# Performance work log

Measured on AMD Instinct MI355X. Metric: run time of the kernel, lower is better.

## Reference

```python
import jax, jax.numpy as jnp
import numpy as np

N = 50000      # nodes
E = 800000     # edges (before self-loops)
HEADS = 4
IN = 128
HID = 96
DH = HID // HEADS  # 24 per-head channels
G = 64         # graphs in batch
OUT = 3


def setup_inputs() -> dict:
    key = jax.random.key(0)
    ks = jax.random.split(key, 16)
    def w(k, shape, fan):
        return (jax.random.normal(k, shape, jnp.float32) * (fan ** -0.5)).astype(jnp.float32)
    x = jax.random.normal(ks[0], (N, IN), jnp.float32)
    edge_index = jax.random.randint(ks[1], (2, E), 0, N, dtype=jnp.int32)
    batch = jnp.sort(jax.random.randint(ks[2], (N,), 0, G, dtype=jnp.int32))
    return {
        'x': x, 'edge_index': edge_index, 'batch': batch, 'num_graphs': G,
        'W1': w(ks[3], (IN, HID), IN),
        'att_src1': w(ks[4], (HEADS, DH), DH),
        'att_dst1': w(ks[5], (HEADS, DH), DH),
        'b1': jnp.zeros((HID,), jnp.float32),
        'W2': w(ks[6], (HID, HID), HID),
        'att_src2': w(ks[7], (HEADS, DH), DH),
        'att_dst2': w(ks[8], (HEADS, DH), DH),
        'b2': jnp.zeros((HID,), jnp.float32),
        'g_w1': w(ks[9], (HID, HID // 2), HID),
        'g_b1': jnp.zeros((HID // 2,), jnp.float32),
        'g_w2': w(ks[10], (HID // 2, 1), HID // 2),
        'g_b2': jnp.zeros((1,), jnp.float32),
        'f_w1': w(ks[11], (HID, HID), HID),
        'f_b1': jnp.zeros((HID,), jnp.float32),
        'f_w2': w(ks[12], (HID, OUT), HID),
        'f_b2': jnp.zeros((OUT,), jnp.float32),
    }


def _gat_layer(x, src, dst, W, a_src, a_dst, b, n):
    # x: [n, F]; src/dst: [E'] (self-loops included). PyG GATConv math.
    h = (x @ W).reshape(n, HEADS, DH)                 # [n, H, d]
    alpha_s = jnp.sum(h * a_src[None], axis=-1)       # [n, H]
    alpha_d = jnp.sum(h * a_dst[None], axis=-1)       # [n, H]
    e = jax.nn.leaky_relu(alpha_s[src] + alpha_d[dst], 0.2)  # [E', H]
    # segment softmax over incoming edges of each dst node
    m = jax.ops.segment_max(e, dst, num_segments=n)   # [n, H]
    ex = jnp.exp(e - m[dst])
    denom = jax.ops.segment_sum(ex, dst, num_segments=n)
    alpha = ex / (denom[dst] + 1e-16)                 # [E', H]
    msg = h[src] * alpha[:, :, None]                  # [E', H, d]
    out = jax.ops.segment_sum(msg, dst, num_segments=n)
    return out.reshape(n, HEADS * DH) + b


def reference(x, edge_index, batch, num_graphs, W1, att_src1, att_dst1, b1,
              W2, att_src2, att_dst2, b2, g_w1, g_b1, g_w2, g_b2,
              f_w1, f_b1, f_w2, f_b2):
    n = x.shape[0]
    loops = jnp.arange(n, dtype=edge_index.dtype)
    src = jnp.concatenate([edge_index[0], loops])     # add self-loops (PyG default)
    dst = jnp.concatenate([edge_index[1], loops])
    h = jax.nn.elu(_gat_layer(x, src, dst, W1, att_src1, att_dst1, b1, n))
    h = jax.nn.elu(_gat_layer(h, src, dst, W2, att_src2, att_dst2, b2, n))
    # GlobalAttention pool: gate_nn -> softmax over batch segments -> weighted sum
    gate = (jax.nn.relu(h @ g_w1 + g_b1) @ g_w2 + g_b2)[:, 0]   # [n]
    gm = jax.ops.segment_max(gate, batch, num_segments=num_graphs)
    gm = jnp.where(jnp.isfinite(gm), gm, 0.0)
    ge = jnp.exp(gate - gm[batch])
    gden = jax.ops.segment_sum(ge, batch, num_segments=num_graphs)
    wgt = ge / (gden[batch] + 1e-16)                  # [n]
    pooled = jax.ops.segment_sum(h * wgt[:, None], batch, num_segments=num_graphs)  # [G, HID]
    return jax.nn.relu(pooled @ f_w1 + f_b1) @ f_w2 + f_b2   # [G, 3]
```

## Files before the change

kernel.cpp:

```cpp
#include <hip/hip_runtime.h>
#include <cmath>

typedef unsigned int uint32;

__device__ __forceinline__ uint32 pack_bf16x2(float a, float b) {
    uint32 ua = __float_as_uint(a), ub = __float_as_uint(b);
    ua = (ua + 0x7fffu + ((ua >> 16) & 1u)) >> 16;
    ub = (ub + 0x7fffu + ((ub >> 16) & 1u)) >> 16;
    return ua | (ub << 16);
}

template<int K, int NCOL, int TN, int MODE>
__device__ __forceinline__ void gemm_body(int bid, const float* __restrict__ X,
                                          const float* __restrict__ W,
                                          const float* __restrict__ v1,
                                          const float* __restrict__ v2,
                                          const float* __restrict__ v3,
                                          uint32* __restrict__ H16, float* __restrict__ Hf,
                                          float* __restrict__ AS, float* __restrict__ AD,
                                          int n_nodes) {
    const int t = threadIdx.x;
    const int tx = t & 15, ty = t >> 4;
    const int c0 = tx * TN;
    const int m0 = ty * 4;
    const int node0 = bid * 64;

    __shared__ float As[16][68];
    __shared__ float Bs[16][NCOL];

    float acc[4][TN];
#pragma unroll
    for (int i = 0; i < 4; i++)
#pragma unroll
        for (int j = 0; j < TN; j++) acc[i][j] = 0.f;

    const int am = t >> 2, akq = t & 3;

    for (int kb = 0; kb < K; kb += 16) {
        float4 av = make_float4(0.f, 0.f, 0.f, 0.f);
        int anode = node0 + am;
        if (anode < n_nodes)
            av = *reinterpret_cast<const float4*>(X + (size_t)anode * K + kb + akq * 4);
        As[akq * 4 + 0][am] = av.x;
        As[akq * 4 + 1][am] = av.y;
        As[akq * 4 + 2][am] = av.z;
        As[akq * 4 + 3][am] = av.w;
        {
            const float4* wsrc = reinterpret_cast<const float4*>(W + (size_t)kb * NCOL);
            float4* bdst = reinterpret_cast<float4*>(&Bs[0][0]);
            for (int i = t; i < 16 * NCOL / 4; i += 256) bdst[i] = wsrc[i];
        }
        __syncthreads();
#pragma unroll
        for (int k = 0; k < 16; k++) {
            float4 a4 = *reinterpret_cast<const float4*>(&As[k][m0]);
            float a[4] = {a4.x, a4.y, a4.z, a4.w};
            float b[TN];
            if constexpr ((TN & 1) == 0) {
#pragma unroll
                for (int j = 0; j < TN / 2; j++) {
                    float2 b2 = *reinterpret_cast<const float2*>(&Bs[k][c0 + 2 * j]);
                    b[2 * j] = b2.x; b[2 * j + 1] = b2.y;
                }
            } else {
#pragma unroll
                for (int j = 0; j < TN; j++) b[j] = Bs[k][c0 + j];
            }
#pragma unroll
            for (int i = 0; i < 4; i++)
#pragma unroll
                for (int j = 0; j < TN; j++)
                    acc[i][j] = fmaf(a[i], b[j], acc[i][j]);
        }
        __syncthreads();
    }

    if constexpr (MODE == 0) {
        __shared__ float s_as[64][16];
        __shared__ float s_ad[64][16];
#pragma unroll
        for (int i = 0; i < 4; i++) {
            int node = node0 + m0 + i;
            float asp = 0.f, adp = 0.f;
#pragma unroll
            for (int j = 0; j < TN; j++) {
                asp = fmaf(acc[i][j], v1[c0 + j], asp);
                adp = fmaf(acc[i][j], v2[c0 + j], adp);
            }
            s_as[m0 + i][tx] = asp;
            s_ad[m0 + i][tx] = adp;
            if (node < n_nodes) {
#pragma unroll
                for (int j = 0; j < TN / 2; j++) {
                    H16[(size_t)node * 48 + tx * (TN / 2) + j] =
                        pack_bf16x2(acc[i][2 * j], acc[i][2 * j + 1]);
                }
            }
        }
        __syncthreads();
        int m = t >> 2, head = t & 3;
        int node = node0 + m;
        if (node < n_nodes) {
            float s1 = s_as[m][head * 4 + 0] + s_as[m][head * 4 + 1]
                     + s_as[m][head * 4 + 2] + s_as[m][head * 4 + 3];
            float s2 = s_ad[m][head * 4 + 0] + s_ad[m][head * 4 + 1]
                     + s_ad[m][head * 4 + 2] + s_ad[m][head * 4 + 3];
            AS[(size_t)node * 4 + head] = s1;
            AD[(size_t)node * 4 + head] = s2;
        }
    } else {
        __shared__ float s_g[64][16];
#pragma unroll
        for (int i = 0; i < 4; i++) {
            float p = 0.f;
#pragma unroll
            for (int j = 0; j < TN; j++) {
                float a = acc[i][j] + v1[c0 + j];
                a = fmaxf(a, 0.f);
                p = fmaf(a, v2[c0 + j], p);
            }
            s_g[m0 + i][tx] = p;
        }
        __syncthreads();
        if (t < 64) {
            int node = node0 + t;
            if (node < n_nodes) {
                float s = 0.f;
#pragma unroll
                for (int j = 0; j < 16; j++) s += s_g[t][j];
                Hf[node] = s + v3[0];
            }
        }
    }
}

template<int K, int NCOL, int TN, int MODE>
__global__ __launch_bounds__(256)
void tiled_gemm_kernel(const float* __restrict__ X, const float* __restrict__ W,
                       const float* __restrict__ v1, const float* __restrict__ v2,
                       const float* __restrict__ v3,
                       uint32* __restrict__ H16, float* __restrict__ Hf,
                       float* __restrict__ AS, float* __restrict__ AD, int n_nodes) {
    gemm_body<K, NCOL, TN, MODE>(blockIdx.x, X, W, v1, v2, v3, H16, Hf, AS, AD, n_nodes);
}

template<int K, int NCOL, int TN>
__global__ __launch_bounds__(256)
void gemm_hist_kernel(const float* __restrict__ X, const float* __restrict__ W,
                      const float* __restrict__ v1, const float* __restrict__ v2,
                      uint32* __restrict__ H16, float* __restrict__ AS, float* __restrict__ AD,
                      int n_nodes, int nb_gemm,
                      const int* __restrict__ dst, int* __restrict__ deg, int E) {
    if ((int)blockIdx.x < nb_gemm) {
        gemm_body<K, NCOL, TN, 0>(blockIdx.x, X, W, v1, v2, nullptr, H16, nullptr,
                                  AS, AD, n_nodes);
    } else {
        int tid = (blockIdx.x - nb_gemm) * 256 + threadIdx.x;
        int stride = (gridDim.x - nb_gemm) * 256;
        for (int e = tid; e < E; e += stride) atomicAdd(&deg[dst[e]], 1);
    }
}

__global__ void scan_bsum_kernel(const int* __restrict__ deg, int* __restrict__ bsum, int n) {
    __shared__ int s[256];
    int t = threadIdx.x;
    int base = blockIdx.x * 1024;
    int sum = 0;
#pragma unroll
    for (int j = 0; j < 4; j++) {
        int i = base + j * 256 + t;
        if (i < n) sum += deg[i] + 1;
    }
    s[t] = sum;
    __syncthreads();
    for (int off = 128; off; off >>= 1) {
        if (t < off) s[t] += s[t + off];
        __syncthreads();
    }
    if (t == 0) bsum[blockIdx.x] = s[0];
}

__global__ void scan_local_kernel(const int* __restrict__ deg, const int* __restrict__ bsum,
                                  int nb, int* __restrict__ rowptr, int* __restrict__ pos,
                                  int n) {
    __shared__ int s[256];
    __shared__ int boff[257];
    int t = threadIdx.x;
    if (t < nb) boff[t] = bsum[t];
    __syncthreads();
    if (t == 0) {
        int run = 0;
        for (int i = 0; i < nb; i++) { int v = boff[i]; boff[i] = run; run += v; }
        boff[nb] = run;
    }
    __syncthreads();
    if (blockIdx.x == 0 && t == 0) rowptr[n] = boff[nb];

    int base = blockIdx.x * 1024;
    int d[4];
    int sum = 0;
#pragma unroll
    for (int j = 0; j < 4; j++) {
        int i = base + t * 4 + j;
        d[j] = (i < n) ? deg[i] + 1 : 0;
        sum += d[j];
    }
    s[t] = sum;
    __syncthreads();
    for (int off = 1; off < 256; off <<= 1) {
        int x = (t >= off) ? s[t - off] : 0;
        __syncthreads();
        s[t] += x;
        __syncthreads();
    }
    int run = boff[blockIdx.x] + s[t] - sum;
#pragma unroll
    for (int j = 0; j < 4; j++) {
        int i = base + t * 4 + j;
        if (i < n) { rowptr[i] = run; pos[i] = run; }
        run += d[j];
    }
}

__global__ void fill_kernel(const int* __restrict__ src, const int* __restrict__ dst,
                            int* __restrict__ pos, int* __restrict__ col, int E, int N) {
    int i = blockIdx.x * blockDim.x + threadIdx.x;
    if (i < E) {
        int p = atomicAdd(&pos[dst[i]], 1);
        col[p] = src[i];
    } else if (i < E + N) {
        int n = i - E;
        int p = atomicAdd(&pos[n], 1);
        col[p] = n;
    }
}

__global__ __launch_bounds__(256)
void gat_gather_kernel(const uint32* __restrict__ H16, const float* __restrict__ AS,
                       const float* __restrict__ AD, const int* __restrict__ rowptr,
                       const int* __restrict__ col, const float* __restrict__ bias,
                       float* __restrict__ OUT, int n_nodes) {
    int wid = threadIdx.x >> 6, lane = threadIdx.x & 63;
    int n = blockIdx.x * 4 + wid;
    if (n >= n_nodes) return;
    int beg = rowptr[n], end = rowptr[n + 1];

    int h = lane & 3, slot = lane >> 2;
    float ad_n = AD[(size_t)n * 4 + h];

    int c = lane;
    bool cown = c < 48;
    int head_c = cown ? (c / 12) : 0;
    const uint32* __restrict__ Hc = H16 + c;

    float denom = 0.f;
    float2 acc0 = make_float2(0.f, 0.f), acc1 = make_float2(0.f, 0.f);
    float2 acc2 = make_float2(0.f, 0.f), acc3 = make_float2(0.f, 0.f);
    float2 acc4 = make_float2(0.f, 0.f), acc5 = make_float2(0.f, 0.f);
    float2 acc6 = make_float2(0.f, 0.f), acc7 = make_float2(0.f, 0.f);

    for (int base = beg; base < end; base += 16) {
        int ce = base + slot;
        int s_e = 0;
        float ex = 0.f;
        if (ce < end) {
            s_e = col[ce];
            float v = AS[(size_t)s_e * 4 + h] + ad_n;
            v = v > 0.f ? v : 0.2f * v;
            ex = __expf(v);
        }
        denom += ex;
        int cnt = end - base;

        int sbv[16];
        float wv[16];
#pragma unroll
        for (int i = 0; i < 16; i++) {
            sbv[i] = __shfl(s_e, i * 4, 64);
            wv[i]  = __shfl(ex,  i * 4 + head_c, 64);
        }

#pragma unroll
        for (int g = 0; g < 16; g += 8) {
            if (g < cnt && cown) {
                uint32 u0 = Hc[(size_t)sbv[g + 0] * 48];
                uint32 u1 = Hc[(size_t)sbv[g + 1] * 48];
                uint32 u2 = Hc[(size_t)sbv[g + 2] * 48];
                uint32 u3 = Hc[(size_t)sbv[g + 3] * 48];
                uint32 u4 = Hc[(size_t)sbv[g + 4] * 48];
                uint32 u5 = Hc[(size_t)sbv[g + 5] * 48];
                uint32 u6 = Hc[(size_t)sbv[g + 6] * 48];
                uint32 u7 = Hc[(size_t)sbv[g + 7] * 48];
                acc0.x = fmaf(__uint_as_float(u0 << 16), wv[g + 0], acc0.x);
                acc0.y = fmaf(__uint_as_float(u0 & 0xffff0000u), wv[g + 0], acc0.y);
                acc1.x = fmaf(__uint_as_float(u1 << 16), wv[g + 1], acc1.x);
                acc1.y = fmaf(__uint_as_float(u1 & 0xffff0000u), wv[g + 1], acc1.y);
                acc2.x = fmaf(__uint_as_float(u2 << 16), wv[g + 2], acc2.x);
                acc2.y = fmaf(__uint_as_float(u2 & 0xffff0000u), wv[g + 2], acc2.y);
                acc3.x = fmaf(__uint_as_float(u3 << 16), wv[g + 3], acc3.x);
                acc3.y = fmaf(__uint_as_float(u3 & 0xffff0000u), wv[g + 3], acc3.y);
                acc4.x = fmaf(__uint_as_float(u4 << 16), wv[g + 4], acc4.x);
                acc4.y = fmaf(__uint_as_float(u4 & 0xffff0000u), wv[g + 4], acc4.y);
                acc5.x = fmaf(__uint_as_float(u5 << 16), wv[g + 5], acc5.x);
                acc5.y = fmaf(__uint_as_float(u5 & 0xffff0000u), wv[g + 5], acc5.y);
                acc6.x = fmaf(__uint_as_float(u6 << 16), wv[g + 6], acc6.x);
                acc6.y = fmaf(__uint_as_float(u6 & 0xffff0000u), wv[g + 6], acc6.y);
                acc7.x = fmaf(__uint_as_float(u7 << 16), wv[g + 7], acc7.x);
                acc7.y = fmaf(__uint_as_float(u7 & 0xffff0000u), wv[g + 7], acc7.y);
            }
        }
    }

#pragma unroll
    for (int m = 4; m <= 32; m <<= 1)
        denom += __shfl_xor(denom, m, 64);
    float den = __shfl(denom, head_c, 64);

    if (cown) {
        float2 a;
        a.x = ((acc0.x + acc1.x) + (acc2.x + acc3.x)) + ((acc4.x + acc5.x) + (acc6.x + acc7.x));
        a.y = ((acc0.y + acc1.y) + (acc2.y + acc3.y)) + ((acc4.y + acc5.y) + (acc6.y + acc7.y));
        float2 b2 = reinterpret_cast<const float2*>(bias)[c];
        float inv = 1.f / (den + 1e-16f);
        float ox = a.x * inv + b2.x;
        float oy = a.y * inv + b2.y;
        ox = ox > 0.f ? ox : (__expf(ox) - 1.f);
        oy = oy > 0.f ? oy : (__expf(oy) - 1.f);
        reinterpret_cast<float2*>(OUT)[(size_t)n * 48 + c] = make_float2(ox, oy);
    }
}

__global__ __launch_bounds__(384)
void pool_accum_kernel(const float* __restrict__ H2, const float* __restrict__ gate,
                       const int* __restrict__ batch, int n_nodes,
                       float* __restrict__ pooled, float* __restrict__ denp) {
    const int NPB = 256;
    int t = threadIdx.x;
    int group = t / 96;
    int c = t - group * 96;
    if (group >= 4) return;
    int nbeg = blockIdx.x * NPB;
    int nend = min(nbeg + NPB, n_nodes);

    float acc = 0.f, dacc = 0.f;
    int curg = -1;
    for (int i = nbeg + group; i < nend; i += 4) {
        int g = batch[i];
        if (g != curg) {
            if (curg >= 0) {
                atomicAdd(&pooled[(size_t)curg * 96 + c], acc);
                if (c == 0) atomicAdd(&denp[curg], dacc);
            }
            acc = 0.f; dacc = 0.f;
            curg = g;
        }
        float ge = __expf(gate[i]);
        acc = fmaf(ge, H2[(size_t)i * 96 + c], acc);
        if (c == 0) dacc += ge;
    }
    if (curg >= 0) {
        atomicAdd(&pooled[(size_t)curg * 96 + c], acc);
        if (c == 0) atomicAdd(&denp[curg], dacc);
    }
}

__global__ void final_kernel(const float* __restrict__ pooled, const float* __restrict__ denp,
                             const float* __restrict__ f_w1, const float* __restrict__ f_b1,
                             const float* __restrict__ f_w2, const float* __restrict__ f_b2,
                             float* __restrict__ out) {
    int g = blockIdx.x, t = threadIdx.x;
    __shared__ float sp[96], sh[96];
    sp[t] = pooled[(size_t)g * 96 + t] / (denp[g] + 1e-16f);
    __syncthreads();
    float a = f_b1[t];
    for (int k = 0; k < 96; k++) a = fmaf(sp[k], f_w1[k * 96 + t], a);
    sh[t] = fmaxf(a, 0.f);
    __syncthreads();
    if (t < 3) {
        float o = f_b2[t];
        for (int k = 0; k < 96; k++) o = fmaf(sh[k], f_w2[k * 3 + t], o);
        out[g * 3 + t] = o;
    }
}

extern "C" void kernel_launch(void* const* d_in, const int* in_sizes, int n_in,
                              void* d_out, int out_size, void* d_ws, size_t ws_size,
                              hipStream_t stream) {
    const float* x    = (const float*)d_in[0];
    const int*   ei   = (const int*)d_in[1];
    const int*   batch= (const int*)d_in[2];
    const float* W1   = (const float*)d_in[4];
    const float* as1  = (const float*)d_in[5];
    const float* ad1  = (const float*)d_in[6];
    const float* b1   = (const float*)d_in[7];
    const float* W2   = (const float*)d_in[8];
    const float* as2  = (const float*)d_in[9];
    const float* ad2  = (const float*)d_in[10];
    const float* b2   = (const float*)d_in[11];
    const float* g_w1 = (const float*)d_in[12];
    const float* g_b1 = (const float*)d_in[13];
    const float* g_w2 = (const float*)d_in[14];
    const float* g_b2 = (const float*)d_in[15];
    const float* f_w1 = (const float*)d_in[16];
    const float* f_b1 = (const float*)d_in[17];
    const float* f_w2 = (const float*)d_in[18];
    const float* f_b2 = (const float*)d_in[19];
    float* out = (float*)d_out;

    int N = in_sizes[0] / 128;
    int E = in_sizes[1] / 2;
    int G = out_size / 3;
    const int* srcv = ei;
    const int* dstv = ei + E;

    char* base = (char*)d_ws;
    int*   deg    = (int*)base;
    float* pooled = (float*)(base + (size_t)N * 4);
    float* denp   = (float*)(base + (size_t)N * 4 + (size_t)G * 96 * 4);
    size_t zbytes = (size_t)(N + G * 96 + G) * 4;

    char* p = base + ((zbytes + 255) & ~(size_t)255);
    auto alloc = [&](size_t bytes) {
        char* q = p;
        p += (bytes + 255) & ~(size_t)255;
        return q;
    };
    uint32* hA   = (uint32*)alloc((size_t)N * 48 * 4);
    float* hB    = (float*)alloc((size_t)N * 96 * 4);
    float* AS    = (float*)alloc((size_t)N * 4 * 4);
    float* AD    = (float*)alloc((size_t)N * 4 * 4);
    float* gatev = (float*)alloc((size_t)N * 4);
    int*   pos   = (int*)alloc((size_t)N * 4);
    int*   rowptr= (int*)alloc(((size_t)N + 1) * 4);
    int*   bsum  = (int*)alloc((size_t)256 * 4);
    int*   col   = (int*)alloc((size_t)(E + N) * 4);

    const int B = 256;
    int gemm_blocks = (N + 63) / 64;
    int nb_scan = (N + 1023) / 1024;

    hipMemsetAsync(base, 0, zbytes, stream);

    gemm_hist_kernel<128, 96, 6><<<gemm_blocks + 256, 256, 0, stream>>>(
        x, W1, as1, ad1, hA, AS, AD, N, gemm_blocks, dstv, deg, E);

    scan_bsum_kernel<<<nb_scan, 256, 0, stream>>>(deg, bsum, N);
    scan_local_kernel<<<nb_scan, 256, 0, stream>>>(deg, bsum, nb_scan, rowptr, pos, N);
    fill_kernel<<<(E + N + B - 1) / B, B, 0, stream>>>(srcv, dstv, pos, col, E, N);

    gat_gather_kernel<<<(N + 3) / 4, 256, 0, stream>>>(hA, AS, AD, rowptr, col, b1, hB, N);
    tiled_gemm_kernel<96, 96, 6, 0><<<gemm_blocks, 256, 0, stream>>>(
        hB, W2, as2, ad2, nullptr, hA, nullptr, AS, AD, N);
    gat_gather_kernel<<<(N + 3) / 4, 256, 0, stream>>>(hA, AS, AD, rowptr, col, b2, hB, N);

    tiled_gemm_kernel<96, 48, 3, 1><<<gemm_blocks, 256, 0, stream>>>(
        hB, g_w1, g_b1, g_w2, g_b2, nullptr, gatev, nullptr, nullptr, N);
    pool_accum_kernel<<<(N + 255) / 256, 384, 0, stream>>>(
        hB, gatev, batch, N, pooled, denp);
    final_kernel<<<G, 96, 0, stream>>>(pooled, denp, f_w1, f_b1, f_w2, f_b2, out);
}
```

Baseline: 302.0 us.

## Fuse gate MLP into second GAT gather and widen per-lane feature loads

The separate gate GEMM kernel is removed. Its 96x48 MLP, ReLU and dot-product reduction now run per node inside the second gather kernel, reading the node's output row from shared memory, which saves a kernel launch and a re-read of the hidden matrix. The gather is also reorganised so each lane loads 8 bytes (4 bf16 channels) per edge, with lane pairs splitting even and odd edges and combining their sums by a shuffle. The trade-off is that the fused gate costs each wave a serial 96-step loop with uncoalesced-per-lane loads of gW1 on every node, which may lengthen the gather kernel.

```diff
diff --git a/kernel.cpp b/kernel.cpp
--- a/kernel.cpp
+++ b/kernel.cpp
@@ -10,13 +10,12 @@
     return ua | (ub << 16);
 }
 
-template<int K, int NCOL, int TN, int MODE>
+template<int K, int NCOL, int TN>
 __device__ __forceinline__ void gemm_body(int bid, const float* __restrict__ X,
                                           const float* __restrict__ W,
                                           const float* __restrict__ v1,
                                           const float* __restrict__ v2,
-                                          const float* __restrict__ v3,
-                                          uint32* __restrict__ H16, float* __restrict__ Hf,
+                                          uint32* __restrict__ H16,
                                           float* __restrict__ AS, float* __restrict__ AD,
                                           int n_nodes) {
     const int t = threadIdx.x;
@@ -56,15 +55,10 @@
             float4 a4 = *reinterpret_cast<const float4*>(&As[k][m0]);
             float a[4] = {a4.x, a4.y, a4.z, a4.w};
             float b[TN];
-            if constexpr ((TN & 1) == 0) {
-#pragma unroll
-                for (int j = 0; j < TN / 2; j++) {
-                    float2 b2 = *reinterpret_cast<const float2*>(&Bs[k][c0 + 2 * j]);
-                    b[2 * j] = b2.x; b[2 * j + 1] = b2.y;
-                }
-            } else {
-#pragma unroll
-                for (int j = 0; j < TN; j++) b[j] = Bs[k][c0 + j];
+#pragma unroll
+            for (int j = 0; j < TN / 2; j++) {
+                float2 b2 = *reinterpret_cast<const float2*>(&Bs[k][c0 + 2 * j]);
+                b[2 * j] = b2.x; b[2 * j + 1] = b2.y;
             }
 #pragma unroll
             for (int i = 0; i < 4; i++)
@@ -75,73 +69,47 @@
         __syncthreads();
     }
 
-    if constexpr (MODE == 0) {
-        __shared__ float s_as[64][16];
-        __shared__ float s_ad[64][16];
-#pragma unroll
-        for (int i = 0; i < 4; i++) {
-            int node = node0 + m0 + i;
-            float asp = 0.f, adp = 0.f;
-#pragma unroll
-            for (int j = 0; j < TN; j++) {
-                asp = fmaf(acc[i][j], v1[c0 + j], asp);
-                adp = fmaf(acc[i][j], v2[c0 + j], adp);
+    __shared__ float s_as[64][16];
+    __shared__ float s_ad[64][16];
+#pragma unroll
+    for (int i = 0; i < 4; i++) {
+        int node = node0 + m0 + i;
+        float asp = 0.f, adp = 0.f;
+#pragma unroll
+        for (int j = 0; j < TN; j++) {
+            asp = fmaf(acc[i][j], v1[c0 + j], asp);
+            adp = fmaf(acc[i][j], v2[c0 + j], adp);
+        }
+        s_as[m0 + i][tx] = asp;
+        s_ad[m0 + i][tx] = adp;
+        if (node < n_nodes) {
+#pragma unroll
+            for (int j = 0; j < TN / 2; j++) {
+                H16[(size_t)node * 48 + tx * (TN / 2) + j] =
+                    pack_bf16x2(acc[i][2 * j], acc[i][2 * j + 1]);
             }
-            s_as[m0 + i][tx] = asp;
-            s_ad[m0 + i][tx] = adp;
-            if (node < n_nodes) {
-#pragma unroll
-                for (int j = 0; j < TN / 2; j++) {
-                    H16[(size_t)node * 48 + tx * (TN / 2) + j] =
-                        pack_bf16x2(acc[i][2 * j], acc[i][2 * j + 1]);
-                }
-            }
-        }
-        __syncthreads();
-        int m = t >> 2, head = t & 3;
-        int node = node0 + m;
-        if (node < n_nodes) {
-            float s1 = s_as[m][head * 4 + 0] + s_as[m][head * 4 + 1]
-                     + s_as[m][head * 4 + 2] + s_as[m][head * 4 + 3];
-            float s2 = s_ad[m][head * 4 + 0] + s_ad[m][head * 4 + 1]
-                     + s_ad[m][head * 4 + 2] + s_ad[m][head * 4 + 3];
-            AS[(size_t)node * 4 + head] = s1;
-            AD[(size_t)node * 4 + head] = s2;
-        }
-    } else {
-        __shared__ float s_g[64][16];
-#pragma unroll
-        for (int i = 0; i < 4; i++) {
-            float p = 0.f;
-#pragma unroll
-            for (int j = 0; j < TN; j++) {
-                float a = acc[i][j] + v1[c0 + j];
-                a = fmaxf(a, 0.f);
-                p = fmaf(a, v2[c0 + j], p);
-            }
-            s_g[m0 + i][tx] = p;
-        }
-        __syncthreads();
-        if (t < 64) {
-            int node = node0 + t;
-            if (node < n_nodes) {
-                float s = 0.f;
-#pragma unroll
-                for (int j = 0; j < 16; j++) s += s_g[t][j];
-                Hf[node] = s + v3[0];
-            }
-        }
-    }
-}
-
-template<int K, int NCOL, int TN, int MODE>
+        }
+    }
+    __syncthreads();
+    int m = t >> 2, head = t & 3;
+    int node = node0 + m;
+    if (node < n_nodes) {
+        float s1 = s_as[m][head * 4 + 0] + s_as[m][head * 4 + 1]
+                 + s_as[m][head * 4 + 2] + s_as[m][head * 4 + 3];
+        float s2 = s_ad[m][head * 4 + 0] + s_ad[m][head * 4 + 1]
+                 + s_ad[m][head * 4 + 2] + s_ad[m][head * 4 + 3];
+        AS[(size_t)node * 4 + head] = s1;
+        AD[(size_t)node * 4 + head] = s2;
+    }
+}
+
+template<int K, int NCOL, int TN>
 __global__ __launch_bounds__(256)
 void tiled_gemm_kernel(const float* __restrict__ X, const float* __restrict__ W,
                        const float* __restrict__ v1, const float* __restrict__ v2,
-                       const float* __restrict__ v3,
-                       uint32* __restrict__ H16, float* __restrict__ Hf,
-                       float* __restrict__ AS, float* __restrict__ AD, int n_nodes) {
-    gemm_body<K, NCOL, TN, MODE>(blockIdx.x, X, W, v1, v2, v3, H16, Hf, AS, AD, n_nodes);
+                       uint32* __restrict__ H16, float* __restrict__ AS,
+                       float* __restrict__ AD, int n_nodes) {
+    gemm_body<K, NCOL, TN>(blockIdx.x, X, W, v1, v2, H16, AS, AD, n_nodes);
 }
 
 template<int K, int NCOL, int TN>
@@ -152,8 +120,7 @@
                       int n_nodes, int nb_gemm,
                       const int* __restrict__ dst, int* __restrict__ deg, int E) {
     if ((int)blockIdx.x < nb_gemm) {
-        gemm_body<K, NCOL, TN, 0>(blockIdx.x, X, W, v1, v2, nullptr, H16, nullptr,
-                                  AS, AD, n_nodes);
+        gemm_body<K, NCOL, TN>(blockIdx.x, X, W, v1, v2, H16, AS, AD, n_nodes);
     } else {
         int tid = (blockIdx.x - nb_gemm) * 256 + threadIdx.x;
         int stride = (gridDim.x - nb_gemm) * 256;
@@ -235,11 +202,16 @@
     }
 }
 
+template<bool GATE>
 __global__ __launch_bounds__(256)
 void gat_gather_kernel(const uint32* __restrict__ H16, const float* __restrict__ AS,
                        const float* __restrict__ AD, const int* __restrict__ rowptr,
                        const int* __restrict__ col, const float* __restrict__ bias,
-                       float* __restrict__ OUT, int n_nodes) {
+                       float* __restrict__ OUT, int n_nodes,
+                       const float* __restrict__ gW1, const float* __restrict__ gb1,
+                       const float* __restrict__ gw2, const float* __restrict__ gb2,
+                       float* __restrict__ gatev) {
+    __shared__ float sh_h[4][96];
     int wid = threadIdx.x >> 6, lane = threadIdx.x & 63;
     int n = blockIdx.x * 4 + wid;
     if (n >= n_nodes) return;
@@ -248,16 +220,13 @@
     int h = lane & 3, slot = lane >> 2;
     float ad_n = AD[(size_t)n * 4 + h];
 
-    int c = lane;
-    bool cown = c < 48;
-    int head_c = cown ? (c / 12) : 0;
-    const uint32* __restrict__ Hc = H16 + c;
+    int pe = lane & 1, q = lane >> 1;
+    bool cown = lane < 48;
+    int head_q = cown ? (q / 6) : 0;
+    const uint2* __restrict__ Hq = reinterpret_cast<const uint2*>(H16) + (cown ? q : 0);
 
     float denom = 0.f;
-    float2 acc0 = make_float2(0.f, 0.f), acc1 = make_float2(0.f, 0.f);
-    float2 acc2 = make_float2(0.f, 0.f), acc3 = make_float2(0.f, 0.f);
-    float2 acc4 = make_float2(0.f, 0.f), acc5 = make_float2(0.f, 0.f);
-    float2 acc6 = make_float2(0.f, 0.f), acc7 = make_float2(0.f, 0.f);
+    float4 acc0 = make_float4(0.f, 0.f, 0.f, 0.f), acc1 = acc0, acc2 = acc0, acc3 = acc0;
 
     for (int base = beg; base < end; base += 16) {
         int ce = base + slot;
@@ -272,41 +241,38 @@
         denom += ex;
         int cnt = end - base;
 
-        int sbv[16];
-        float wv[16];
-#pragma unroll
-        for (int i = 0; i < 16; i++) {
-            sbv[i] = __shfl(s_e, i * 4, 64);
-            wv[i]  = __shfl(ex,  i * 4 + head_c, 64);
-        }
-
-#pragma unroll
-        for (int g = 0; g < 16; g += 8) {
-            if (g < cnt && cown) {
-                uint32 u0 = Hc[(size_t)sbv[g + 0] * 48];
-                uint32 u1 = Hc[(size_t)sbv[g + 1] * 48];
-                uint32 u2 = Hc[(size_t)sbv[g + 2] * 48];
-                uint32 u3 = Hc[(size_t)sbv[g + 3] * 48];
-                uint32 u4 = Hc[(size_t)sbv[g + 4] * 48];
-                uint32 u5 = Hc[(size_t)sbv[g + 5] * 48];
-                uint32 u6 = Hc[(size_t)sbv[g + 6] * 48];
-                uint32 u7 = Hc[(size_t)sbv[g + 7] * 48];
-                acc0.x = fmaf(__uint_as_float(u0 << 16), wv[g + 0], acc0.x);
-                acc0.y = fmaf(__uint_as_float(u0 & 0xffff0000u), wv[g + 0], acc0.y);
-                acc1.x = fmaf(__uint_as_float(u1 << 16), wv[g + 1], acc1.x);
-                acc1.y = fmaf(__uint_as_float(u1 & 0xffff0000u), wv[g + 1], acc1.y);
-                acc2.x = fmaf(__uint_as_float(u2 << 16), wv[g + 2], acc2.x);
-                acc2.y = fmaf(__uint_as_float(u2 & 0xffff0000u), wv[g + 2], acc2.y);
-                acc3.x = fmaf(__uint_as_float(u3 << 16), wv[g + 3], acc3.x);
-                acc3.y = fmaf(__uint_as_float(u3 & 0xffff0000u), wv[g + 3], acc3.y);
-                acc4.x = fmaf(__uint_as_float(u4 << 16), wv[g + 4], acc4.x);
-                acc4.y = fmaf(__uint_as_float(u4 & 0xffff0000u), wv[g + 4], acc4.y);
-                acc5.x = fmaf(__uint_as_float(u5 << 16), wv[g + 5], acc5.x);
-                acc5.y = fmaf(__uint_as_float(u5 & 0xffff0000u), wv[g + 5], acc5.y);
-                acc6.x = fmaf(__uint_as_float(u6 << 16), wv[g + 6], acc6.x);
-                acc6.y = fmaf(__uint_as_float(u6 & 0xffff0000u), wv[g + 6], acc6.y);
-                acc7.x = fmaf(__uint_as_float(u7 << 16), wv[g + 7], acc7.x);
-                acc7.y = fmaf(__uint_as_float(u7 & 0xffff0000u), wv[g + 7], acc7.y);
+        int sb[8];
+        float w[8];
+#pragma unroll
+        for (int j = 0; j < 8; j++) {
+            int esel = 2 * j + pe;
+            sb[j] = __shfl(s_e, esel * 4, 64);
+            w[j]  = __shfl(ex,  esel * 4 + head_q, 64);
+        }
+
+#pragma unroll
+        for (int g = 0; g < 8; g += 4) {
+            if (2 * g < cnt && cown) {
+                uint2 u0 = Hq[(size_t)sb[g + 0] * 24];
+                uint2 u1 = Hq[(size_t)sb[g + 1] * 24];
+                uint2 u2 = Hq[(size_t)sb[g + 2] * 24];
+                uint2 u3 = Hq[(size_t)sb[g + 3] * 24];
+                acc0.x = fmaf(__uint_as_float(u0.x << 16),        w[g + 0], acc0.x);
+                acc0.y = fmaf(__uint_as_float(u0.x & 0xffff0000u), w[g + 0], acc0.y);
+                acc0.z = fmaf(__uint_as_float(u0.y << 16),        w[g + 0], acc0.z);
+                acc0.w = fmaf(__uint_as_float(u0.y & 0xffff0000u), w[g + 0], acc0.w);
+                acc1.x = fmaf(__uint_as_float(u1.x << 16),        w[g + 1], acc1.x);
+                acc1.y = fmaf(__uint_as_float(u1.x & 0xffff0000u), w[g + 1], acc1.y);
+                acc1.z = fmaf(__uint_as_float(u1.y << 16),        w[g + 1], acc1.z);
+                acc1.w = fmaf(__uint_as_float(u1.y & 0xffff0000u), w[g + 1], acc1.w);
+                acc2.x = fmaf(__uint_as_float(u2.x << 16),        w[g + 2], acc2.x);
+                acc2.y = fmaf(__uint_as_float(u2.x & 0xffff0000u), w[g + 2], acc2.y);
+                acc2.z = fmaf(__uint_as_float(u2.y << 16),        w[g + 2], acc2.z);
+                acc2.w = fmaf(__uint_as_float(u2.y & 0xffff0000u), w[g + 2], acc2.w);
+                acc3.x = fmaf(__uint_as_float(u3.x << 16),        w[g + 3], acc3.x);
+                acc3.y = fmaf(__uint_as_float(u3.x & 0xffff0000u), w[g + 3], acc3.y);
+                acc3.z = fmaf(__uint_as_float(u3.y << 16),        w[g + 3], acc3.z);
+                acc3.w = fmaf(__uint_as_float(u3.y & 0xffff0000u), w[g + 3], acc3.w);
             }
         }
     }
@@ -314,19 +280,48 @@
 #pragma unroll
     for (int m = 4; m <= 32; m <<= 1)
         denom += __shfl_xor(denom, m, 64);
-    float den = __shfl(denom, head_c, 64);
-
-    if (cown) {
-        float2 a;
-        a.x = ((acc0.x + acc1.x) + (acc2.x + acc3.x)) + ((acc4.x + acc5.x) + (acc6.x + acc7.x));
-        a.y = ((acc0.y + acc1.y) + (acc2.y + acc3.y)) + ((acc4.y + acc5.y) + (acc6.y + acc7.y));
-        float2 b2 = reinterpret_cast<const float2*>(bias)[c];
+    float den = __shfl(denom, head_q, 64);
+
+    float4 a;
+    a.x = (acc0.x + acc1.x) + (acc2.x + acc3.x);
+    a.y = (acc0.y + acc1.y) + (acc2.y + acc3.y);
+    a.z = (acc0.z + acc1.z) + (acc2.z + acc3.z);
+    a.w = (acc0.w + acc1.w) + (acc2.w + acc3.w);
+    a.x += __shfl_xor(a.x, 1, 64);
+    a.y += __shfl_xor(a.y, 1, 64);
+    a.z += __shfl_xor(a.z, 1, 64);
+    a.w += __shfl_xor(a.w, 1, 64);
+
+    if (cown && pe == 0) {
         float inv = 1.f / (den + 1e-16f);
-        float ox = a.x * inv + b2.x;
-        float oy = a.y * inv + b2.y;
-        ox = ox > 0.f ? ox : (__expf(ox) - 1.f);
-        oy = oy > 0.f ? oy : (__expf(oy) - 1.f);
-        reinterpret_cast<float2*>(OUT)[(size_t)n * 48 + c] = make_float2(ox, oy);
+        float4 b4 = reinterpret_cast<const float4*>(bias)[q];
+        float4 o;
+        o.x = a.x * inv + b4.x;
+        o.y = a.y * inv + b4.y;
+        o.z = a.z * inv + b4.z;
+        o.w = a.w * inv + b4.w;
+        o.x = o.x > 0.f ? o.x : (__expf(o.x) - 1.f);
+        o.y = o.y > 0.f ? o.y : (__expf(o.y) - 1.f);
+        o.z = o.z > 0.f ? o.z : (__expf(o.z) - 1.f);
+        o.w = o.w > 0.f ? o.w : (__expf(o.w) - 1.f);
+        reinterpret_cast<float4*>(OUT)[(size_t)n * 24 + q] = o;
+        if (GATE) *reinterpret_cast<float4*>(&sh_h[wid][4 * q]) = o;
+    }
+
+    if (GATE) {
+        __builtin_amdgcn_wave_barrier();
+        float gv = 0.f;
+        if (lane < 48) {
+            float aj = gb1[lane];
+            for (int cc = 0; cc < 96; cc++)
+                aj = fmaf(sh_h[wid][cc], gW1[cc * 48 + lane], aj);
+            aj = fmaxf(aj, 0.f);
+            gv = aj * gw2[lane];
+        }
+#pragma unroll
+        for (int m = 1; m <= 32; m <<= 1)
+            gv += __shfl_xor(gv, m, 64);
+        if (lane == 0) gatev[n] = gv + gb2[0];
     }
 }
 
@@ -448,13 +443,13 @@
     scan_local_kernel<<<nb_scan, 256, 0, stream>>>(deg, bsum, nb_scan, rowptr, pos, N);
     fill_kernel<<<(E + N + B - 1) / B, B, 0, stream>>>(srcv, dstv, pos, col, E, N);
 
-    gat_gather_kernel<<<(N + 3) / 4, 256, 0, stream>>>(hA, AS, AD, rowptr, col, b1, hB, N);
-    tiled_gemm_kernel<96, 96, 6, 0><<<gemm_blocks, 256, 0, stream>>>(
-        hB, W2, as2, ad2, nullptr, hA, nullptr, AS, AD, N);
-    gat_gather_kernel<<<(N + 3) / 4, 256, 0, stream>>>(hA, AS, AD, rowptr, col, b2, hB, N);
-
-    tiled_gemm_kernel<96, 48, 3, 1><<<gemm_blocks, 256, 0, stream>>>(
-        hB, g_w1, g_b1, g_w2, g_b2, nullptr, gatev, nullptr, nullptr, N);
+    gat_gather_kernel<false><<<(N + 3) / 4, 256, 0, stream>>>(
+        hA, AS, AD, rowptr, col, b1, hB, N, nullptr, nullptr, nullptr, nullptr, nullptr);
+    tiled_gemm_kernel<96, 96, 6><<<gemm_blocks, 256, 0, stream>>>(
+        hB, W2, as2, ad2, hA, AS, AD, N);
+    gat_gather_kernel<true><<<(N + 3) / 4, 256, 0, stream>>>(
+        hA, AS, AD, rowptr, col, b2, hB, N, g_w1, g_b1, g_w2, g_b2, gatev);
+
     pool_accum_kernel<<<(N + 255) / 256, 384, 0, stream>>>(
         hB, gatev, batch, N, pooled, denp);
     final_kernel<<<G, 96, 0, stream>>>(pooled, denp, f_w1, f_b1, f_w2, f_b2, out);
```

Measured after the change: 305.5 us. About the same (+1.2%).
